# Optimization experiments

Hardware: AMD Instinct MI355X
Metric: run time of the kernel (lower is better)

Reference implementation:

```python
import jax, jax.numpy as jnp
import numpy as np

# irreps_in = irreps_out = 32x0e + 16x1o ; irreps_sh = 1x0e + 1x1o
MUL0, MUL1 = 32, 16
N_NODES = 12000
N_EDGES = 120000
INV_SQRT3 = float(1.0 / np.sqrt(3.0))   # w3j(1,1,0), w3j(0,1,1), w3j(1,0,1) coefficient
SQRT2 = float(np.sqrt(2.0))             # e3nn normalize2mom constant for ReLU
# e3nn TP norms: irrep_normalization='component', path_normalization='element'.
# Each output irrep receives paths with num_elements 32 and 16 -> x = 48.
N_0E = float(1.0 / np.sqrt(48.0))       # alpha = dim(0e)/48 = 1/48
N_1O = float(np.sqrt(3.0 / 48.0))       # alpha = dim(1o)/48 = 3/48
# uvw weight blocks (mul2 = 1): (s,y0->s),(s,y0->g),(v,y1->s),(v,y1->g),(s,y1->v),(v,y0->v)
SPLITS = [MUL0 * MUL0, MUL0 * MUL1, MUL1 * MUL0, MUL1 * MUL1, MUL0 * MUL1, MUL1 * MUL1]
OFFS = np.cumsum([0] + SPLITS)
WNUM = int(OFFS[-1])  # 3072


def setup_inputs() -> dict:
    key = jax.random.key(0)
    k1, k2, k3, k4, k5 = jax.random.split(key, 5)
    x = jax.random.normal(k1, (N_NODES, MUL0 + 3 * MUL1), dtype=jnp.float32)
    edge_attr = jax.random.normal(k2, (N_EDGES, 64), dtype=jnp.float32)
    Yij = jax.random.normal(k3, (N_EDGES, 4), dtype=jnp.float32)
    edge_index = jax.random.randint(k4, (2, N_EDGES), 0, N_NODES, dtype=jnp.int64)
    w_emb = jax.random.normal(k5, (2 * MUL0 + 64, WNUM), dtype=jnp.float32)
    return {"x": x, "edge_attr": edge_attr, "Yij": Yij,
            "edge_index": edge_index, "w_emb": w_emb}


def reference(x, edge_attr, Yij, edge_index, w_emb):
    dst, src = edge_index[0], edge_index[1]
    E = edge_attr.shape[0]
    xs = x[:, :MUL0]                                   # [N, 32] scalars (0e)
    xv = x[:, MUL0:].reshape(-1, MUL1, 3)              # [N, 16, 3] vectors (1o)

    # per-edge weight MLP (single e3nn FC layer, weight scaled by 1/sqrt(fan_in))
    emb = jnp.concatenate([xs[dst], xs[src], edge_attr], axis=-1)     # [E, 128]
    w = emb @ (w_emb / np.sqrt(w_emb.shape[0]))                       # [E, 3072]
    Ws = [w[:, OFFS[i]:OFFS[i + 1]] for i in range(6)]
    W1 = Ws[0].reshape(E, MUL0, MUL0)
    W2 = Ws[1].reshape(E, MUL0, MUL1)
    W3 = Ws[2].reshape(E, MUL1, MUL0)
    W4 = Ws[3].reshape(E, MUL1, MUL1)
    W5 = Ws[4].reshape(E, MUL0, MUL1)
    W6 = Ws[5].reshape(E, MUL1, MUL1)

    # gather source features, split sh
    x1s, x1v = xs[src], xv[src]                        # [E,32], [E,16,3]
    y0, y1 = Yij[:, 0], Yij[:, 1:4]                    # [E], [E,3]

    sy0 = x1s * y0[:, None]                            # 0e x 0e paths
    vdot = jnp.einsum('euk,ek->eu', x1v, y1) * INV_SQRT3  # 1o x 1o -> 0e
    out_s = N_0E * (jnp.einsum('euw,eu->ew', W1, sy0) +
                    jnp.einsum('euw,eu->ew', W3, vdot))    # [E, 32]
    out_g = N_0E * (jnp.einsum('euw,eu->ew', W2, sy0) +
                    jnp.einsum('euw,eu->ew', W4, vdot))    # [E, 16]
    out_v = (N_1O * INV_SQRT3) * (
        jnp.einsum('euw,eu,ek->ewk', W5, x1s, y1) +
        jnp.einsum('euw,euk->ewk', W6, x1v * y0[:, None, None]))  # [E, 16, 3]

    msg = jnp.concatenate([out_s, out_g, out_v.reshape(E, MUL1 * 3)], axis=-1)  # [E, 96]

    # scatter mean onto destination nodes
    summed = jax.ops.segment_sum(msg, dst, num_segments=N_NODES)
    cnt = jax.ops.segment_sum(jnp.ones((E,), msg.dtype), dst, num_segments=N_NODES)
    mean = summed / jnp.maximum(cnt, 1.0)[:, None]

    # Gate (e3nn Activation normalizes ReLU by sqrt(2))
    s = SQRT2 * jax.nn.relu(mean[:, :MUL0])
    g = SQRT2 * jax.nn.relu(mean[:, MUL0:MUL0 + MUL1])
    v = mean[:, MUL0 + MUL1:].reshape(-1, MUL1, 3) * g[:, :, None]
    out = jnp.concatenate([s, v.reshape(-1, MUL1 * 3)], axis=-1)     # [N, 80]
    return x + out
```

## Files before the change

### kernel.cpp

```cpp
#include <hip/hip_runtime.h>
#include <hip/hip_bf16.h>

#define E_EDGES 120000
#define NUM_NODES 12000

typedef __attribute__((ext_vector_type(8))) short bfrag;
typedef __attribute__((ext_vector_type(8))) unsigned short ushort8;
typedef __attribute__((ext_vector_type(4))) float f32x4;

#define INV_SQRT3 0.57735026918962576f
#define SQRT2_C   1.41421356237309515f
#define N_0E_C    0.14433756729740643f
#define NV_C      0.14433756729740643f
#define WSCALE    0.08838834764831845f

__device__ __forceinline__ unsigned short f2bf(float f) {
    union { float f; unsigned int u; } v; v.f = f;
    unsigned int r = v.u + 0x7fffu + ((v.u >> 16) & 1u);
    return (unsigned short)(r >> 16);
}

__device__ __forceinline__ ushort8 pack8(f32x4 a, f32x4 b) {
    ushort8 o;
    o[0] = f2bf(a.x); o[1] = f2bf(a.y); o[2] = f2bf(a.z); o[3] = f2bf(a.w);
    o[4] = f2bf(b.x); o[5] = f2bf(b.y); o[6] = f2bf(b.z); o[7] = f2bf(b.w);
    return o;
}

__global__ void k_wt(const float* __restrict__ w_emb, unsigned short* __restrict__ Bt) {
    int o = blockIdx.x * 256 + threadIdx.x;
    if (o >= 3072 * 128) return;
    int t = o >> 11;
    int c = (o >> 3) & 255;
    int j = o & 7;
    int kb = c >> 6;
    int quad = (c >> 4) & 3;
    int col = c & 15;
    int k = kb * 32 + quad * 8 + j;
    int n = t * 16 + col;
    Bt[o] = f2bf(w_emb[k * 3072 + n] * WSCALE);
}

__global__ void k_prep(const float* __restrict__ x, const float* __restrict__ edge_attr,
                       const float* __restrict__ Yij, const int* __restrict__ edge_index,
                       unsigned short* __restrict__ emb, float* __restrict__ rT,
                       float* __restrict__ cnt) {
    int e = blockIdx.x * 256 + threadIdx.x;
    if (e >= E_EDGES) return;
    int dst = edge_index[e];
    int src = edge_index[E_EDGES + e];
    f32x4 y = *(const f32x4*)(Yij + 4 * (long)e);
    float y0 = y.x, y1a = y.y, y1b = y.z, y1c = y.w;
    const float* xd = x + (long)dst * 80;
    const float* xs = x + (long)src * 80;
    const float* ea = edge_attr + (long)e * 64;

    ushort8* embp = (ushort8*)(emb + (long)e * 128);

    float xsv[80];
#pragma unroll
    for (int i = 0; i < 80; i += 4) {
        f32x4 v = *(const f32x4*)(xs + i);
        xsv[i] = v.x; xsv[i + 1] = v.y; xsv[i + 2] = v.z; xsv[i + 3] = v.w;
    }
#pragma unroll
    for (int cb = 0; cb < 4; ++cb) {
        f32x4 a = *(const f32x4*)(xd + cb * 8);
        f32x4 b = *(const f32x4*)(xd + cb * 8 + 4);
        embp[cb] = pack8(a, b);
    }
#pragma unroll
    for (int cb = 0; cb < 4; ++cb) {
        f32x4 a, b;
        a.x = xsv[cb * 8 + 0]; a.y = xsv[cb * 8 + 1]; a.z = xsv[cb * 8 + 2]; a.w = xsv[cb * 8 + 3];
        b.x = xsv[cb * 8 + 4]; b.y = xsv[cb * 8 + 5]; b.z = xsv[cb * 8 + 6]; b.w = xsv[cb * 8 + 7];
        embp[4 + cb] = pack8(a, b);
    }
#pragma unroll
    for (int cb = 0; cb < 8; ++cb) {
        f32x4 a = *(const f32x4*)(ea + cb * 8);
        f32x4 b = *(const f32x4*)(ea + cb * 8 + 4);
        embp[8 + cb] = pack8(a, b);
    }
#pragma unroll
    for (int u = 0; u < 32; ++u) rT[(long)u * E_EDGES + e] = xsv[u] * y0;
#pragma unroll
    for (int u = 0; u < 16; ++u)
        rT[(long)(32 + u) * E_EDGES + e] =
            (xsv[32 + 3 * u] * y1a + xsv[33 + 3 * u] * y1b + xsv[34 + 3 * u] * y1c) * INV_SQRT3;
#pragma unroll
    for (int u = 0; u < 32; ++u) rT[(long)(48 + u) * E_EDGES + e] = xsv[u];
#pragma unroll
    for (int j = 0; j < 48; ++j) rT[(long)(80 + j) * E_EDGES + e] = xsv[32 + j] * y0;
    atomicAdd(cnt + dst, 1.0f);
}

__global__ __launch_bounds__(256, 4) void k_gemm(
    const unsigned short* __restrict__ emb, const unsigned short* __restrict__ Bt,
    const float* __restrict__ rT, const int* __restrict__ edge_index,
    const float* __restrict__ Yij, float* __restrict__ summed) {
    const int lane = threadIdx.x & 63;
    const int wave = threadIdx.x >> 6;
    long e0 = (long)blockIdx.x * 128 + (long)wave * 32;
    const bool dup = (e0 + 32 > E_EDGES);
    if (dup) e0 = E_EDGES - 32;
    const int col = lane & 15, quad = lane >> 4;

    __shared__ __align__(16) char lds[2][16384];

    bfrag A[2][4];
#pragma unroll
    for (int s = 0; s < 2; ++s) {
        const unsigned short* ap = emb + (e0 + s * 16 + col) * 128 + quad * 8;
#pragma unroll
        for (int kb = 0; kb < 4; ++kb) A[s][kb] = *(const bfrag*)(ap + kb * 32);
    }

    auto stage = [&](int ci) {
        const char* g = (const char*)Bt + (size_t)ci * 16384 + wave * 4096 + lane * 16;
        char* l = &lds[ci & 1][wave * 4096];
#pragma unroll
        for (int j = 0; j < 4; ++j)
            __builtin_amdgcn_global_load_lds(
                (const __attribute__((address_space(1))) unsigned int*)(g + j * 1024),
                (__attribute__((address_space(3))) unsigned int*)(l + j * 1024), 16, 0, 0);
    };

    f32x4 z = {0.f, 0.f, 0.f, 0.f};
    f32x4 acc_s0[2] = {z, z}, acc_s1[2] = {z, z}, acc_g[2] = {z, z}, acc_t5[2] = {z, z};
    f32x4 acc_v[2][3] = {{z, z, z}, {z, z, z}};

    const float* rbase = rT + e0 + quad * 4;
    auto loadw = [&](int r, f32x4& a, f32x4& b) {
        const float* p = rbase + (long)r * E_EDGES;
        a = *(const f32x4*)(p);
        b = *(const f32x4*)(p + 16);
    };

    auto tile = [&](const char* lt, f32x4& c0, f32x4& c1) {
        bfrag B0 = *(const bfrag*)(lt + lane * 16);
        bfrag B1 = *(const bfrag*)(lt + lane * 16 + 1024);
        bfrag B2 = *(const bfrag*)(lt + lane * 16 + 2048);
        bfrag B3 = *(const bfrag*)(lt + lane * 16 + 3072);
        c0 = z; c1 = z;
        c0 = __builtin_amdgcn_mfma_f32_16x16x32_bf16(A[0][0], B0, c0, 0, 0, 0);
        c1 = __builtin_amdgcn_mfma_f32_16x16x32_bf16(A[1][0], B0, c1, 0, 0, 0);
        c0 = __builtin_amdgcn_mfma_f32_16x16x32_bf16(A[0][1], B1, c0, 0, 0, 0);
        c1 = __builtin_amdgcn_mfma_f32_16x16x32_bf16(A[1][1], B1, c1, 0, 0, 0);
        c0 = __builtin_amdgcn_mfma_f32_16x16x32_bf16(A[0][2], B2, c0, 0, 0, 0);
        c1 = __builtin_amdgcn_mfma_f32_16x16x32_bf16(A[1][2], B2, c1, 0, 0, 0);
        c0 = __builtin_amdgcn_mfma_f32_16x16x32_bf16(A[0][3], B3, c0, 0, 0, 0);
        c1 = __builtin_amdgcn_mfma_f32_16x16x32_bf16(A[1][3], B3, c1, 0, 0, 0);
    };

    stage(0);
    int cidx = 0;
    auto nextbuf = [&]() -> const char* {
        __syncthreads();
        if (cidx + 1 < 48) stage(cidx + 1);
        const char* b = lds[cidx & 1];
        ++cidx;
        return b;
    };

    f32x4 c0, c1;

    {
        f32x4 p0a, p0b, p1a, p1b;
        loadw(0, p0a, p0b); loadw(1, p1a, p1b);
#pragma unroll 1
        for (int j = 0; j < 16; ++j) {
            const char* buf = nextbuf();
            f32x4 w0a = p0a, w0b = p0b, w1a = p1a, w1b = p1b;
            int nr = (j < 15) ? (2 * j + 2) : 0;
            loadw(nr, p0a, p0b); loadw(nr + 1, p1a, p1b);
            tile(buf,         c0, c1); acc_s0[0] += c0 * w0a; acc_s0[1] += c1 * w0b;
            tile(buf + 4096,  c0, c1); acc_s1[0] += c0 * w0a; acc_s1[1] += c1 * w0b;
            tile(buf + 8192,  c0, c1); acc_s0[0] += c0 * w1a; acc_s0[1] += c1 * w1b;
            tile(buf + 12288, c0, c1); acc_s1[0] += c0 * w1a; acc_s1[1] += c1 * w1b;
        }
    }
    {
        f32x4 pa[4], pb[4];
#pragma unroll
        for (int i = 0; i < 4; ++i) loadw(i, pa[i], pb[i]);
#pragma unroll 1
        for (int j = 0; j < 8; ++j) {
            const char* buf = nextbuf();
            f32x4 wa[4], wb[4];
#pragma unroll
            for (int i = 0; i < 4; ++i) { wa[i] = pa[i]; wb[i] = pb[i]; }
            int nr = (j < 7) ? (4 * j + 4) : 0;
#pragma unroll
            for (int i = 0; i < 4; ++i) loadw(nr + i, pa[i], pb[i]);
#pragma unroll
            for (int i = 0; i < 4; ++i) {
                tile(buf + i * 4096, c0, c1);
                acc_g[0] += c0 * wa[i]; acc_g[1] += c1 * wb[i];
            }
        }
    }
    {
        f32x4 p0a, p0b, p1a, p1b;
        loadw(32, p0a, p0b); loadw(33, p1a, p1b);
#pragma unroll 1
        for (int j = 0; j < 8; ++j) {
            const char* buf = nextbuf();
            f32x4 w0a = p0a, w0b = p0b, w1a = p1a, w1b = p1b;
            int nr = (j < 7) ? (32 + 2 * j + 2) : 32;
            loadw(nr, p0a, p0b); loadw(nr + 1, p1a, p1b);
            tile(buf,         c0, c1); acc_s0[0] += c0 * w0a; acc_s0[1] += c1 * w0b;
            tile(buf + 4096,  c0, c1); acc_s1[0] += c0 * w0a; acc_s1[1] += c1 * w0b;
            tile(buf + 8192,  c0, c1); acc_s0[0] += c0 * w1a; acc_s0[1] += c1 * w1b;
            tile(buf + 12288, c0, c1); acc_s1[0] += c0 * w1a; acc_s1[1] += c1 * w1b;
        }
    }
    {
        f32x4 pa[4], pb[4];
#pragma unroll
        for (int i = 0; i < 4; ++i) loadw(32 + i, pa[i], pb[i]);
#pragma unroll 1
        for (int j = 0; j < 4; ++j) {
            const char* buf = nextbuf();
            f32x4 wa[4], wb[4];
#pragma unroll
            for (int i = 0; i < 4; ++i) { wa[i] = pa[i]; wb[i] = pb[i]; }
            int nr = (j < 3) ? (32 + 4 * j + 4) : 32;
#pragma unroll
            for (int i = 0; i < 4; ++i) loadw(nr + i, pa[i], pb[i]);
#pragma unroll
            for (int i = 0; i < 4; ++i) {
                tile(buf + i * 4096, c0, c1);
                acc_g[0] += c0 * wa[i]; acc_g[1] += c1 * wb[i];
            }
        }
    }
    {
        f32x4 pa[4], pb[4];
#pragma unroll
        for (int i = 0; i < 4; ++i) loadw(48 + i, pa[i], pb[i]);
#pragma unroll 1
        for (int j = 0; j < 8; ++j) {
            const char* buf = nextbuf();
            f32x4 wa[4], wb[4];
#pragma unroll
            for (int i = 0; i < 4; ++i) { wa[i] = pa[i]; wb[i] = pb[i]; }
            int nr = (j < 7) ? (48 + 4 * j + 4) : 48;
#pragma unroll
            for (int i = 0; i < 4; ++i) loadw(nr + i, pa[i], pb[i]);
#pragma unroll
            for (int i = 0; i < 4; ++i) {
                tile(buf + i * 4096, c0, c1);
                acc_t5[0] += c0 * wa[i]; acc_t5[1] += c1 * wb[i];
            }
        }
    }
    {
        f32x4 va[3], vb[3];
#pragma unroll
        for (int k = 0; k < 3; ++k) loadw(80 + k, va[k], vb[k]);
#pragma unroll 1
        for (int j = 0; j < 4; ++j) {
            const char* buf = nextbuf();
#pragma unroll
            for (int i = 0; i < 4; ++i) {
                f32x4 wa[3], wb[3];
#pragma unroll
                for (int k = 0; k < 3; ++k) { wa[k] = va[k]; wb[k] = vb[k]; }
                int un = 4 * j + i + 1; if (un > 15) un = 0;
#pragma unroll
                for (int k = 0; k < 3; ++k) loadw(80 + 3 * un + k, va[k], vb[k]);
                tile(buf + i * 4096, c0, c1);
#pragma unroll
                for (int k = 0; k < 3; ++k) {
                    acc_v[0][k] += c0 * wa[k];
                    acc_v[1][k] += c1 * wb[k];
                }
            }
        }
    }

    if (dup) return;
#pragma unroll
    for (int s = 0; s < 2; ++s) {
        long eb = e0 + s * 16 + quad * 4;
#pragma unroll
        for (int r = 0; r < 4; ++r) {
            long e = eb + r;
            int d = edge_index[e];
            float* base = summed + (long)d * 96;
            float y1a = Yij[4 * e + 1], y1b = Yij[4 * e + 2], y1c = Yij[4 * e + 3];
            atomicAdd(base + col,       N_0E_C * acc_s0[s][r]);
            atomicAdd(base + col + 16,  N_0E_C * acc_s1[s][r]);
            atomicAdd(base + 32 + col,  N_0E_C * acc_g[s][r]);
            float t5 = acc_t5[s][r];
            atomicAdd(base + 48 + col * 3 + 0, NV_C * (t5 * y1a + acc_v[s][0][r]));
            atomicAdd(base + 48 + col * 3 + 1, NV_C * (t5 * y1b + acc_v[s][1][r]));
            atomicAdd(base + 48 + col * 3 + 2, NV_C * (t5 * y1c + acc_v[s][2][r]));
        }
    }
}

__global__ void k_final(const float* __restrict__ x, const float* __restrict__ summed,
                        const float* __restrict__ cnt, float* __restrict__ out) {
    int tid = blockIdx.x * 256 + threadIdx.x;
    if (tid >= NUM_NODES * 80) return;
    int n = tid / 80, c = tid % 80;
    float m = fmaxf(cnt[n], 1.0f);
    float inv = 1.0f / m;
    float val;
    if (c < 32) {
        val = SQRT2_C * fmaxf(summed[(long)n * 96 + c] * inv, 0.0f);
    } else {
        int j = c - 32;
        int w = j / 3;
        float g = SQRT2_C * fmaxf(summed[(long)n * 96 + 32 + w] * inv, 0.0f);
        val = summed[(long)n * 96 + 48 + j] * inv * g;
    }
    out[tid] = x[tid] + val;
}

extern "C" void kernel_launch(void* const* d_in, const int* in_sizes, int n_in,
                              void* d_out, int out_size, void* d_ws, size_t ws_size,
                              hipStream_t stream) {
    const float* x         = (const float*)d_in[0];
    const float* edge_attr = (const float*)d_in[1];
    const float* Yij       = (const float*)d_in[2];
    const int*   edge_index= (const int*)d_in[3];
    const float* w_emb     = (const float*)d_in[4];
    float* out = (float*)d_out;

    char* ws = (char*)d_ws;
    size_t off = 0;
    unsigned short* emb = (unsigned short*)(ws + off); off += (size_t)E_EDGES * 128 * 2;
    unsigned short* Bt  = (unsigned short*)(ws + off); off += (size_t)3072 * 128 * 2;
    off = (off + 255) & ~(size_t)255;
    float* rT     = (float*)(ws + off); off += (size_t)128 * E_EDGES * 4;
    size_t zoff = off;
    float* summed = (float*)(ws + off); off += (size_t)NUM_NODES * 96 * 4;
    float* cnt    = (float*)(ws + off); off += (size_t)NUM_NODES * 4;

    hipMemsetAsync(ws + zoff, 0, (size_t)NUM_NODES * 97 * 4, stream);
    k_wt  <<<(3072 * 128 + 255) / 256, 256, 0, stream>>>(w_emb, Bt);
    k_prep<<<(E_EDGES + 255) / 256, 256, 0, stream>>>(x, edge_attr, Yij, edge_index, emb, rT, cnt);
    k_gemm<<<(E_EDGES + 127) / 128, 256, 0, stream>>>(emb, Bt, rT, edge_index, Yij, summed);
    k_final<<<(NUM_NODES * 80 + 255) / 256, 256, 0, stream>>>(x, summed, cnt, out);
}
```

Before: 299.3 us.

## Factor y0 out of per-edge weights and stage weight rows in LDS

Moves the y0 multiplication out of the precomputed per-edge rows and applies it once per output in the epilogue, using separate accumulators for each weight block. This removes duplicate rows and shrinks the rT buffer from 128 to 96 rows, which cuts both the write traffic in k_prep and the read traffic in k_gemm. Each block now bulk-loads its 96x128 slice of rT into LDS with global_load_lds instead of issuing per-iteration prefetched global loads. The extra 48KB of LDS forces launch bounds down from 4 to 2 blocks per CU, so the kernel has less latency hiding. It also needs more accumulator registers.

Result: slower. 306.1 us (+2.3%).

```diff
diff --git a/kernel.cpp b/kernel.cpp
--- a/kernel.cpp
+++ b/kernel.cpp
@@ -50,7 +50,7 @@
     int dst = edge_index[e];
     int src = edge_index[E_EDGES + e];
     f32x4 y = *(const f32x4*)(Yij + 4 * (long)e);
-    float y0 = y.x, y1a = y.y, y1b = y.z, y1c = y.w;
+    float y1a = y.y, y1b = y.z, y1c = y.w;
     const float* xd = x + (long)dst * 80;
     const float* xs = x + (long)src * 80;
     const float* ea = edge_attr + (long)e * 64;
@@ -83,19 +83,17 @@
         embp[8 + cb] = pack8(a, b);
     }
 #pragma unroll
-    for (int u = 0; u < 32; ++u) rT[(long)u * E_EDGES + e] = xsv[u] * y0;
+    for (int u = 0; u < 32; ++u) rT[(long)u * E_EDGES + e] = xsv[u];
 #pragma unroll
     for (int u = 0; u < 16; ++u)
         rT[(long)(32 + u) * E_EDGES + e] =
             (xsv[32 + 3 * u] * y1a + xsv[33 + 3 * u] * y1b + xsv[34 + 3 * u] * y1c) * INV_SQRT3;
 #pragma unroll
-    for (int u = 0; u < 32; ++u) rT[(long)(48 + u) * E_EDGES + e] = xsv[u];
-#pragma unroll
-    for (int j = 0; j < 48; ++j) rT[(long)(80 + j) * E_EDGES + e] = xsv[32 + j] * y0;
+    for (int j = 0; j < 48; ++j) rT[(long)(48 + j) * E_EDGES + e] = xsv[32 + j];
     atomicAdd(cnt + dst, 1.0f);
 }
 
-__global__ __launch_bounds__(256, 4) void k_gemm(
+__global__ __launch_bounds__(256, 2) void k_gemm(
     const unsigned short* __restrict__ emb, const unsigned short* __restrict__ Bt,
     const float* __restrict__ rT, const int* __restrict__ edge_index,
     const float* __restrict__ Yij, float* __restrict__ summed) {
@@ -107,6 +105,7 @@
     const int col = lane & 15, quad = lane >> 4;
 
     __shared__ __align__(16) char lds[2][16384];
+    __shared__ __align__(16) float wlds[96][128];
 
     bfrag A[2][4];
 #pragma unroll
@@ -114,6 +113,21 @@
         const unsigned short* ap = emb + (e0 + s * 16 + col) * 128 + quad * 8;
 #pragma unroll
         for (int kb = 0; kb < 4; ++kb) A[s][kb] = *(const bfrag*)(ap + kb * 32);
+    }
+
+    {
+#pragma unroll
+        for (int it = 0; it < 12; ++it) {
+            int o = it * 4096 + wave * 1024 + lane * 16;
+            int row = o >> 9;
+            int rb = o & 511;
+            const char* g = (const char*)rT + (size_t)row * ((size_t)E_EDGES * 4)
+                          + (size_t)blockIdx.x * 512 + rb;
+            char* l = (char*)wlds + it * 4096 + wave * 1024;
+            __builtin_amdgcn_global_load_lds(
+                (const __attribute__((address_space(1))) unsigned int*)g,
+                (__attribute__((address_space(3))) unsigned int*)l, 16, 0, 0);
+        }
     }
 
     auto stage = [&](int ci) {
@@ -127,14 +141,16 @@
     };
 
     f32x4 z = {0.f, 0.f, 0.f, 0.f};
-    f32x4 acc_s0[2] = {z, z}, acc_s1[2] = {z, z}, acc_g[2] = {z, z}, acc_t5[2] = {z, z};
+    f32x4 accW1_0[2] = {z, z}, accW1_1[2] = {z, z};
+    f32x4 accW3_0[2] = {z, z}, accW3_1[2] = {z, z};
+    f32x4 accW2[2] = {z, z}, accW4[2] = {z, z};
+    f32x4 acc_t5[2] = {z, z};
     f32x4 acc_v[2][3] = {{z, z, z}, {z, z, z}};
 
-    const float* rbase = rT + e0 + quad * 4;
+    const int woff = wave * 32 + quad * 4;
     auto loadw = [&](int r, f32x4& a, f32x4& b) {
-        const float* p = rbase + (long)r * E_EDGES;
-        a = *(const f32x4*)(p);
-        b = *(const f32x4*)(p + 16);
+        a = *(const f32x4*)&wlds[r][woff];
+        b = *(const f32x4*)&wlds[r][woff + 16];
     };
 
     auto tile = [&](const char* lt, f32x4& c0, f32x4& c1) {
@@ -165,117 +181,67 @@
 
     f32x4 c0, c1;
 
-    {
-        f32x4 p0a, p0b, p1a, p1b;
-        loadw(0, p0a, p0b); loadw(1, p1a, p1b);
-#pragma unroll 1
-        for (int j = 0; j < 16; ++j) {
-            const char* buf = nextbuf();
-            f32x4 w0a = p0a, w0b = p0b, w1a = p1a, w1b = p1b;
-            int nr = (j < 15) ? (2 * j + 2) : 0;
-            loadw(nr, p0a, p0b); loadw(nr + 1, p1a, p1b);
-            tile(buf,         c0, c1); acc_s0[0] += c0 * w0a; acc_s0[1] += c1 * w0b;
-            tile(buf + 4096,  c0, c1); acc_s1[0] += c0 * w0a; acc_s1[1] += c1 * w0b;
-            tile(buf + 8192,  c0, c1); acc_s0[0] += c0 * w1a; acc_s0[1] += c1 * w1b;
-            tile(buf + 12288, c0, c1); acc_s1[0] += c0 * w1a; acc_s1[1] += c1 * w1b;
-        }
-    }
-    {
-        f32x4 pa[4], pb[4];
-#pragma unroll
-        for (int i = 0; i < 4; ++i) loadw(i, pa[i], pb[i]);
-#pragma unroll 1
-        for (int j = 0; j < 8; ++j) {
-            const char* buf = nextbuf();
-            f32x4 wa[4], wb[4];
-#pragma unroll
-            for (int i = 0; i < 4; ++i) { wa[i] = pa[i]; wb[i] = pb[i]; }
-            int nr = (j < 7) ? (4 * j + 4) : 0;
-#pragma unroll
-            for (int i = 0; i < 4; ++i) loadw(nr + i, pa[i], pb[i]);
-#pragma unroll
-            for (int i = 0; i < 4; ++i) {
-                tile(buf + i * 4096, c0, c1);
-                acc_g[0] += c0 * wa[i]; acc_g[1] += c1 * wb[i];
-            }
-        }
-    }
-    {
-        f32x4 p0a, p0b, p1a, p1b;
-        loadw(32, p0a, p0b); loadw(33, p1a, p1b);
-#pragma unroll 1
-        for (int j = 0; j < 8; ++j) {
-            const char* buf = nextbuf();
-            f32x4 w0a = p0a, w0b = p0b, w1a = p1a, w1b = p1b;
-            int nr = (j < 7) ? (32 + 2 * j + 2) : 32;
-            loadw(nr, p0a, p0b); loadw(nr + 1, p1a, p1b);
-            tile(buf,         c0, c1); acc_s0[0] += c0 * w0a; acc_s0[1] += c1 * w0b;
-            tile(buf + 4096,  c0, c1); acc_s1[0] += c0 * w0a; acc_s1[1] += c1 * w0b;
-            tile(buf + 8192,  c0, c1); acc_s0[0] += c0 * w1a; acc_s0[1] += c1 * w1b;
-            tile(buf + 12288, c0, c1); acc_s1[0] += c0 * w1a; acc_s1[1] += c1 * w1b;
-        }
-    }
-    {
-        f32x4 pa[4], pb[4];
-#pragma unroll
-        for (int i = 0; i < 4; ++i) loadw(32 + i, pa[i], pb[i]);
-#pragma unroll 1
-        for (int j = 0; j < 4; ++j) {
-            const char* buf = nextbuf();
-            f32x4 wa[4], wb[4];
-#pragma unroll
-            for (int i = 0; i < 4; ++i) { wa[i] = pa[i]; wb[i] = pb[i]; }
-            int nr = (j < 3) ? (32 + 4 * j + 4) : 32;
-#pragma unroll
-            for (int i = 0; i < 4; ++i) loadw(nr + i, pa[i], pb[i]);
-#pragma unroll
-            for (int i = 0; i < 4; ++i) {
-                tile(buf + i * 4096, c0, c1);
-                acc_g[0] += c0 * wa[i]; acc_g[1] += c1 * wb[i];
-            }
-        }
-    }
-    {
-        f32x4 pa[4], pb[4];
-#pragma unroll
-        for (int i = 0; i < 4; ++i) loadw(48 + i, pa[i], pb[i]);
-#pragma unroll 1
-        for (int j = 0; j < 8; ++j) {
-            const char* buf = nextbuf();
-            f32x4 wa[4], wb[4];
-#pragma unroll
-            for (int i = 0; i < 4; ++i) { wa[i] = pa[i]; wb[i] = pb[i]; }
-            int nr = (j < 7) ? (48 + 4 * j + 4) : 48;
-#pragma unroll
-            for (int i = 0; i < 4; ++i) loadw(nr + i, pa[i], pb[i]);
-#pragma unroll
-            for (int i = 0; i < 4; ++i) {
-                tile(buf + i * 4096, c0, c1);
-                acc_t5[0] += c0 * wa[i]; acc_t5[1] += c1 * wb[i];
-            }
-        }
-    }
-    {
-        f32x4 va[3], vb[3];
-#pragma unroll
-        for (int k = 0; k < 3; ++k) loadw(80 + k, va[k], vb[k]);
-#pragma unroll 1
-        for (int j = 0; j < 4; ++j) {
-            const char* buf = nextbuf();
-#pragma unroll
-            for (int i = 0; i < 4; ++i) {
-                f32x4 wa[3], wb[3];
-#pragma unroll
-                for (int k = 0; k < 3; ++k) { wa[k] = va[k]; wb[k] = vb[k]; }
-                int un = 4 * j + i + 1; if (un > 15) un = 0;
-#pragma unroll
-                for (int k = 0; k < 3; ++k) loadw(80 + 3 * un + k, va[k], vb[k]);
-                tile(buf + i * 4096, c0, c1);
-#pragma unroll
-                for (int k = 0; k < 3; ++k) {
-                    acc_v[0][k] += c0 * wa[k];
-                    acc_v[1][k] += c1 * wb[k];
-                }
+#pragma unroll 1
+    for (int j = 0; j < 16; ++j) {
+        const char* buf = nextbuf();
+        f32x4 w0a, w0b, w1a, w1b;
+        loadw(2 * j, w0a, w0b); loadw(2 * j + 1, w1a, w1b);
+        tile(buf,         c0, c1); accW1_0[0] += c0 * w0a; accW1_0[1] += c1 * w0b;
+        tile(buf + 4096,  c0, c1); accW1_1[0] += c0 * w0a; accW1_1[1] += c1 * w0b;
+        tile(buf + 8192,  c0, c1); accW1_0[0] += c0 * w1a; accW1_0[1] += c1 * w1b;
+        tile(buf + 12288, c0, c1); accW1_1[0] += c0 * w1a; accW1_1[1] += c1 * w1b;
+    }
+#pragma unroll 1
+    for (int j = 0; j < 8; ++j) {
+        const char* buf = nextbuf();
+#pragma unroll
+        for (int i = 0; i < 4; ++i) {
+            f32x4 wa, wb; loadw(4 * j + i, wa, wb);
+            tile(buf + i * 4096, c0, c1);
+            accW2[0] += c0 * wa; accW2[1] += c1 * wb;
+        }
+    }
+#pragma unroll 1
+    for (int j = 0; j < 8; ++j) {
+        const char* buf = nextbuf();
+        f32x4 w0a, w0b, w1a, w1b;
+        loadw(32 + 2 * j, w0a, w0b); loadw(32 + 2 * j + 1, w1a, w1b);
+        tile(buf,         c0, c1); accW3_0[0] += c0 * w0a; accW3_0[1] += c1 * w0b;
+        tile(buf + 4096,  c0, c1); accW3_1[0] += c0 * w0a; accW3_1[1] += c1 * w0b;
+        tile(buf + 8192,  c0, c1); accW3_0[0] += c0 * w1a; accW3_0[1] += c1 * w1b;
+        tile(buf + 12288, c0, c1); accW3_1[0] += c0 * w1a; accW3_1[1] += c1 * w1b;
+    }
+#pragma unroll 1
+    for (int j = 0; j < 4; ++j) {
+        const char* buf = nextbuf();
+#pragma unroll
+        for (int i = 0; i < 4; ++i) {
+            f32x4 wa, wb; loadw(32 + 4 * j + i, wa, wb);
+            tile(buf + i * 4096, c0, c1);
+            accW4[0] += c0 * wa; accW4[1] += c1 * wb;
+        }
+    }
+#pragma unroll 1
+    for (int j = 0; j < 8; ++j) {
+        const char* buf = nextbuf();
+#pragma unroll
+        for (int i = 0; i < 4; ++i) {
+            f32x4 wa, wb; loadw(4 * j + i, wa, wb);
+            tile(buf + i * 4096, c0, c1);
+            acc_t5[0] += c0 * wa; acc_t5[1] += c1 * wb;
+        }
+    }
+#pragma unroll 1
+    for (int j = 0; j < 4; ++j) {
+        const char* buf = nextbuf();
+#pragma unroll
+        for (int i = 0; i < 4; ++i) {
+            int u = 4 * j + i;
+            tile(buf + i * 4096, c0, c1);
+#pragma unroll
+            for (int k = 0; k < 3; ++k) {
+                f32x4 wa, wb; loadw(48 + 3 * u + k, wa, wb);
+                acc_v[0][k] += c0 * wa; acc_v[1][k] += c1 * wb;
             }
         }
     }
@@ -289,14 +255,15 @@
             long e = eb + r;
             int d = edge_index[e];
             float* base = summed + (long)d * 96;
-            float y1a = Yij[4 * e + 1], y1b = Yij[4 * e + 2], y1c = Yij[4 * e + 3];
-            atomicAdd(base + col,       N_0E_C * acc_s0[s][r]);
-            atomicAdd(base + col + 16,  N_0E_C * acc_s1[s][r]);
-            atomicAdd(base + 32 + col,  N_0E_C * acc_g[s][r]);
+            f32x4 y = *(const f32x4*)(Yij + 4 * e);
+            float y0 = y.x, y1a = y.y, y1b = y.z, y1c = y.w;
+            atomicAdd(base + col,      N_0E_C * (y0 * accW1_0[s][r] + accW3_0[s][r]));
+            atomicAdd(base + col + 16, N_0E_C * (y0 * accW1_1[s][r] + accW3_1[s][r]));
+            atomicAdd(base + 32 + col, N_0E_C * (y0 * accW2[s][r] + accW4[s][r]));
             float t5 = acc_t5[s][r];
-            atomicAdd(base + 48 + col * 3 + 0, NV_C * (t5 * y1a + acc_v[s][0][r]));
-            atomicAdd(base + 48 + col * 3 + 1, NV_C * (t5 * y1b + acc_v[s][1][r]));
-            atomicAdd(base + 48 + col * 3 + 2, NV_C * (t5 * y1c + acc_v[s][2][r]));
+            atomicAdd(base + 48 + col * 3 + 0, NV_C * (t5 * y1a + y0 * acc_v[s][0][r]));
+            atomicAdd(base + 48 + col * 3 + 1, NV_C * (t5 * y1b + y0 * acc_v[s][1][r]));
+            atomicAdd(base + 48 + col * 3 + 2, NV_C * (t5 * y1c + y0 * acc_v[s][2][r]));
         }
     }
 }
@@ -335,7 +302,7 @@
     unsigned short* emb = (unsigned short*)(ws + off); off += (size_t)E_EDGES * 128 * 2;
     unsigned short* Bt  = (unsigned short*)(ws + off); off += (size_t)3072 * 128 * 2;
     off = (off + 255) & ~(size_t)255;
-    float* rT     = (float*)(ws + off); off += (size_t)128 * E_EDGES * 4;
+    float* rT     = (float*)(ws + off); off += (size_t)96 * E_EDGES * 4;
     size_t zoff = off;
     float* summed = (float*)(ws + off); off += (size_t)NUM_NODES * 96 * 4;
     float* cnt    = (float*)(ws + off); off += (size_t)NUM_NODES * 4;
```

## Prefetch LDS chunks two ahead with split barriers and MFMA priority

Applied to the files above, without the earlier changes.

Reworks the double-buffered LDS pipeline. Each chunk now waits with a partial vmcnt before one barrier, then re-stages the freed buffer two chunks ahead after a second barrier. The goal is for global-to-LDS copies to overlap more of the MFMA work, instead of a full syncthreads followed immediately by staging. It also raises wave priority around the MFMA tile sections with s_setprio. The price is a second barrier per chunk and hand-tuned waitcnt values that depend on how many loads are in flight.

Result: slower. 449.6 us (+50.2%).

```diff
diff --git a/kernel.cpp b/kernel.cpp
--- a/kernel.cpp
+++ b/kernel.cpp
@@ -153,31 +153,41 @@
         c1 = __builtin_amdgcn_mfma_f32_16x16x32_bf16(A[1][3], B3, c1, 0, 0, 0);
     };
 
+    int cidx = 0;
+    auto chunk_top = [&]() -> const char* {
+        asm volatile("s_waitcnt vmcnt(4)" ::: "memory");
+        __builtin_amdgcn_s_barrier();
+        asm volatile("" ::: "memory");
+        return lds[cidx & 1];
+    };
+    auto chunk_bot = [&]() {
+        __builtin_amdgcn_s_setprio(0);
+        asm volatile("" ::: "memory");
+        __builtin_amdgcn_s_barrier();
+        asm volatile("" ::: "memory");
+        if (cidx + 2 < 48) stage(cidx + 2);
+        ++cidx;
+    };
+
+    f32x4 c0, c1;
+
     stage(0);
-    int cidx = 0;
-    auto nextbuf = [&]() -> const char* {
-        __syncthreads();
-        if (cidx + 1 < 48) stage(cidx + 1);
-        const char* b = lds[cidx & 1];
-        ++cidx;
-        return b;
-    };
-
-    f32x4 c0, c1;
-
     {
         f32x4 p0a, p0b, p1a, p1b;
         loadw(0, p0a, p0b); loadw(1, p1a, p1b);
+        stage(1);
 #pragma unroll 1
         for (int j = 0; j < 16; ++j) {
-            const char* buf = nextbuf();
+            const char* buf = chunk_top();
             f32x4 w0a = p0a, w0b = p0b, w1a = p1a, w1b = p1b;
             int nr = (j < 15) ? (2 * j + 2) : 0;
             loadw(nr, p0a, p0b); loadw(nr + 1, p1a, p1b);
+            __builtin_amdgcn_s_setprio(1);
             tile(buf,         c0, c1); acc_s0[0] += c0 * w0a; acc_s0[1] += c1 * w0b;
             tile(buf + 4096,  c0, c1); acc_s1[0] += c0 * w0a; acc_s1[1] += c1 * w0b;
             tile(buf + 8192,  c0, c1); acc_s0[0] += c0 * w1a; acc_s0[1] += c1 * w1b;
             tile(buf + 12288, c0, c1); acc_s1[0] += c0 * w1a; acc_s1[1] += c1 * w1b;
+            chunk_bot();
         }
     }
     {
@@ -186,18 +196,20 @@
         for (int i = 0; i < 4; ++i) loadw(i, pa[i], pb[i]);
 #pragma unroll 1
         for (int j = 0; j < 8; ++j) {
-            const char* buf = nextbuf();
+            const char* buf = chunk_top();
             f32x4 wa[4], wb[4];
 #pragma unroll
             for (int i = 0; i < 4; ++i) { wa[i] = pa[i]; wb[i] = pb[i]; }
             int nr = (j < 7) ? (4 * j + 4) : 0;
 #pragma unroll
             for (int i = 0; i < 4; ++i) loadw(nr + i, pa[i], pb[i]);
+            __builtin_amdgcn_s_setprio(1);
 #pragma unroll
             for (int i = 0; i < 4; ++i) {
                 tile(buf + i * 4096, c0, c1);
                 acc_g[0] += c0 * wa[i]; acc_g[1] += c1 * wb[i];
             }
+            chunk_bot();
         }
     }
     {
@@ -205,14 +217,16 @@
         loadw(32, p0a, p0b); loadw(33, p1a, p1b);
 #pragma unroll 1
         for (int j = 0; j < 8; ++j) {
-            const char* buf = nextbuf();
+            const char* buf = chunk_top();
             f32x4 w0a = p0a, w0b = p0b, w1a = p1a, w1b = p1b;
             int nr = (j < 7) ? (32 + 2 * j + 2) : 32;
             loadw(nr, p0a, p0b); loadw(nr + 1, p1a, p1b);
+            __builtin_amdgcn_s_setprio(1);
             tile(buf,         c0, c1); acc_s0[0] += c0 * w0a; acc_s0[1] += c1 * w0b;
             tile(buf + 4096,  c0, c1); acc_s1[0] += c0 * w0a; acc_s1[1] += c1 * w0b;
             tile(buf + 8192,  c0, c1); acc_s0[0] += c0 * w1a; acc_s0[1] += c1 * w1b;
             tile(buf + 12288, c0, c1); acc_s1[0] += c0 * w1a; acc_s1[1] += c1 * w1b;
+            chunk_bot();
         }
     }
     {
@@ -221,18 +235,20 @@
         for (int i = 0; i < 4; ++i) loadw(32 + i, pa[i], pb[i]);
 #pragma unroll 1
         for (int j = 0; j < 4; ++j) {
-            const char* buf = nextbuf();
+            const char* buf = chunk_top();
             f32x4 wa[4], wb[4];
 #pragma unroll
             for (int i = 0; i < 4; ++i) { wa[i] = pa[i]; wb[i] = pb[i]; }
             int nr = (j < 3) ? (32 + 4 * j + 4) : 32;
 #pragma unroll
             for (int i = 0; i < 4; ++i) loadw(nr + i, pa[i], pb[i]);
+            __builtin_amdgcn_s_setprio(1);
 #pragma unroll
             for (int i = 0; i < 4; ++i) {
                 tile(buf + i * 4096, c0, c1);
                 acc_g[0] += c0 * wa[i]; acc_g[1] += c1 * wb[i];
             }
+            chunk_bot();
         }
     }
     {
@@ -241,18 +257,20 @@
         for (int i = 0; i < 4; ++i) loadw(48 + i, pa[i], pb[i]);
 #pragma unroll 1
         for (int j = 0; j < 8; ++j) {
-            const char* buf = nextbuf();
+            const char* buf = chunk_top();
             f32x4 wa[4], wb[4];
 #pragma unroll
             for (int i = 0; i < 4; ++i) { wa[i] = pa[i]; wb[i] = pb[i]; }
             int nr = (j < 7) ? (48 + 4 * j + 4) : 48;
 #pragma unroll
             for (int i = 0; i < 4; ++i) loadw(nr + i, pa[i], pb[i]);
+            __builtin_amdgcn_s_setprio(1);
 #pragma unroll
             for (int i = 0; i < 4; ++i) {
                 tile(buf + i * 4096, c0, c1);
                 acc_t5[0] += c0 * wa[i]; acc_t5[1] += c1 * wb[i];
             }
+            chunk_bot();
         }
     }
     {
@@ -261,7 +279,7 @@
         for (int k = 0; k < 3; ++k) loadw(80 + k, va[k], vb[k]);
 #pragma unroll 1
         for (int j = 0; j < 4; ++j) {
-            const char* buf = nextbuf();
+            const char* buf = chunk_top();
 #pragma unroll
             for (int i = 0; i < 4; ++i) {
                 f32x4 wa[3], wb[3];
@@ -270,13 +288,16 @@
                 int un = 4 * j + i + 1; if (un > 15) un = 0;
 #pragma unroll
                 for (int k = 0; k < 3; ++k) loadw(80 + 3 * un + k, va[k], vb[k]);
+                __builtin_amdgcn_s_setprio(1);
                 tile(buf + i * 4096, c0, c1);
 #pragma unroll
                 for (int k = 0; k < 3; ++k) {
                     acc_v[0][k] += c0 * wa[k];
                     acc_v[1][k] += c1 * wb[k];
                 }
+                __builtin_amdgcn_s_setprio(0);
             }
+            chunk_bot();
         }
     }
 
```

## Sort edges by destination and remap gemm blocks per XCD for atomic locality

Applied to the files above, without the earlier changes.

Adds a counting sort of edges by destination node (count, single-block scan, scatter), so prep and gemm process edges in dst-sorted order. The scatter-add atomics into summed then hit contiguous node rows, and consecutive blocks are remapped so each XCD handles a contiguous range of edges, improving L2 locality of the atomics. The cost is three extra small kernels (one of them a serial single-block scan), extra workspace, and gathered reads of edge_attr and Yij via the permutation. Y values are also staged in sorted order for the epilogue.

Result: slower. 450.3 us (+50.5%).

```diff
diff --git a/kernel.cpp b/kernel.cpp
--- a/kernel.cpp
+++ b/kernel.cpp
@@ -41,21 +41,59 @@
     Bt[o] = f2bf(w_emb[k * 3072 + n] * WSCALE);
 }
 
+__global__ void k_count(const int* __restrict__ edge_index, float* __restrict__ cnt) {
+    int e = blockIdx.x * 256 + threadIdx.x;
+    if (e >= E_EDGES) return;
+    atomicAdd(cnt + edge_index[e], 1.0f);
+}
+
+__global__ void k_scan(const float* __restrict__ cnt, int* __restrict__ offs) {
+    __shared__ int psum[256];
+    int t = threadIdx.x;
+    const int SEG = (NUM_NODES + 255) / 256;
+    int lo = t * SEG;
+    int hi = lo + SEG; if (hi > NUM_NODES) hi = NUM_NODES;
+    int s = 0;
+    for (int i = lo; i < hi; ++i) s += (int)cnt[i];
+    psum[t] = s;
+    __syncthreads();
+    if (t == 0) {
+        int acc = 0;
+        for (int i = 0; i < 256; ++i) { int v = psum[i]; psum[i] = acc; acc += v; }
+    }
+    __syncthreads();
+    int acc = psum[t];
+    for (int i = lo; i < hi; ++i) { offs[i] = acc; acc += (int)cnt[i]; }
+}
+
+__global__ void k_scatter(const int* __restrict__ edge_index, const int* __restrict__ offs,
+                          int* __restrict__ cursor, int* __restrict__ perm_src,
+                          int* __restrict__ dsts) {
+    int e = blockIdx.x * 256 + threadIdx.x;
+    if (e >= E_EDGES) return;
+    int d = edge_index[e];
+    int p = offs[d] + atomicAdd(cursor + d, 1);
+    perm_src[p] = e;
+    dsts[p] = d;
+}
+
 __global__ void k_prep(const float* __restrict__ x, const float* __restrict__ edge_attr,
                        const float* __restrict__ Yij, const int* __restrict__ edge_index,
+                       const int* __restrict__ perm_src, const int* __restrict__ dsts,
                        unsigned short* __restrict__ emb, float* __restrict__ rT,
-                       float* __restrict__ cnt) {
-    int e = blockIdx.x * 256 + threadIdx.x;
-    if (e >= E_EDGES) return;
-    int dst = edge_index[e];
-    int src = edge_index[E_EDGES + e];
-    f32x4 y = *(const f32x4*)(Yij + 4 * (long)e);
+                       f32x4* __restrict__ ys) {
+    int p = blockIdx.x * 256 + threadIdx.x;
+    if (p >= E_EDGES) return;
+    int eid = perm_src[p];
+    int dst = dsts[p];
+    int src = edge_index[E_EDGES + eid];
+    f32x4 y = *(const f32x4*)(Yij + 4 * (long)eid);
     float y0 = y.x, y1a = y.y, y1b = y.z, y1c = y.w;
     const float* xd = x + (long)dst * 80;
     const float* xs = x + (long)src * 80;
-    const float* ea = edge_attr + (long)e * 64;
-
-    ushort8* embp = (ushort8*)(emb + (long)e * 128);
+    const float* ea = edge_attr + (long)eid * 64;
+
+    ushort8* embp = (ushort8*)(emb + (long)p * 128);
 
     float xsv[80];
 #pragma unroll
@@ -83,25 +121,30 @@
         embp[8 + cb] = pack8(a, b);
     }
 #pragma unroll
-    for (int u = 0; u < 32; ++u) rT[(long)u * E_EDGES + e] = xsv[u] * y0;
+    for (int u = 0; u < 32; ++u) rT[(long)u * E_EDGES + p] = xsv[u] * y0;
 #pragma unroll
     for (int u = 0; u < 16; ++u)
-        rT[(long)(32 + u) * E_EDGES + e] =
+        rT[(long)(32 + u) * E_EDGES + p] =
             (xsv[32 + 3 * u] * y1a + xsv[33 + 3 * u] * y1b + xsv[34 + 3 * u] * y1c) * INV_SQRT3;
 #pragma unroll
-    for (int u = 0; u < 32; ++u) rT[(long)(48 + u) * E_EDGES + e] = xsv[u];
-#pragma unroll
-    for (int j = 0; j < 48; ++j) rT[(long)(80 + j) * E_EDGES + e] = xsv[32 + j] * y0;
-    atomicAdd(cnt + dst, 1.0f);
+    for (int u = 0; u < 32; ++u) rT[(long)(48 + u) * E_EDGES + p] = xsv[u];
+#pragma unroll
+    for (int j = 0; j < 48; ++j) rT[(long)(80 + j) * E_EDGES + p] = xsv[32 + j] * y0;
+    ys[p] = y;
 }
 
 __global__ __launch_bounds__(256, 4) void k_gemm(
     const unsigned short* __restrict__ emb, const unsigned short* __restrict__ Bt,
-    const float* __restrict__ rT, const int* __restrict__ edge_index,
-    const float* __restrict__ Yij, float* __restrict__ summed) {
+    const float* __restrict__ rT, const int* __restrict__ dsts,
+    const f32x4* __restrict__ ys, float* __restrict__ summed) {
     const int lane = threadIdx.x & 63;
     const int wave = threadIdx.x >> 6;
-    long e0 = (long)blockIdx.x * 128 + (long)wave * 32;
+    const int NB = (E_EDGES + 127) / 128;
+    const int q = NB >> 3, r = NB & 7;
+    int hb = blockIdx.x;
+    int xcd = hb & 7, ii = hb >> 3;
+    int lb = (xcd < r ? xcd * (q + 1) : r * (q + 1) + (xcd - r) * q) + ii;
+    long e0 = (long)lb * 128 + (long)wave * 32;
     const bool dup = (e0 + 32 > E_EDGES);
     if (dup) e0 = E_EDGES - 32;
     const int col = lane & 15, quad = lane >> 4;
@@ -131,8 +174,8 @@
     f32x4 acc_v[2][3] = {{z, z, z}, {z, z, z}};
 
     const float* rbase = rT + e0 + quad * 4;
-    auto loadw = [&](int r, f32x4& a, f32x4& b) {
-        const float* p = rbase + (long)r * E_EDGES;
+    auto loadw = [&](int r_, f32x4& a, f32x4& b) {
+        const float* p = rbase + (long)r_ * E_EDGES;
         a = *(const f32x4*)(p);
         b = *(const f32x4*)(p + 16);
     };
@@ -285,18 +328,19 @@
     for (int s = 0; s < 2; ++s) {
         long eb = e0 + s * 16 + quad * 4;
 #pragma unroll
-        for (int r = 0; r < 4; ++r) {
-            long e = eb + r;
-            int d = edge_index[e];
+        for (int r_ = 0; r_ < 4; ++r_) {
+            long e = eb + r_;
+            int d = dsts[e];
             float* base = summed + (long)d * 96;
-            float y1a = Yij[4 * e + 1], y1b = Yij[4 * e + 2], y1c = Yij[4 * e + 3];
-            atomicAdd(base + col,       N_0E_C * acc_s0[s][r]);
-            atomicAdd(base + col + 16,  N_0E_C * acc_s1[s][r]);
-            atomicAdd(base + 32 + col,  N_0E_C * acc_g[s][r]);
-            float t5 = acc_t5[s][r];
-            atomicAdd(base + 48 + col * 3 + 0, NV_C * (t5 * y1a + acc_v[s][0][r]));
-            atomicAdd(base + 48 + col * 3 + 1, NV_C * (t5 * y1b + acc_v[s][1][r]));
-            atomicAdd(base + 48 + col * 3 + 2, NV_C * (t5 * y1c + acc_v[s][2][r]));
+            f32x4 y = ys[e];
+            float y1a = y.y, y1b = y.z, y1c = y.w;
+            atomicAdd(base + col,       N_0E_C * acc_s0[s][r_]);
+            atomicAdd(base + col + 16,  N_0E_C * acc_s1[s][r_]);
+            atomicAdd(base + 32 + col,  N_0E_C * acc_g[s][r_]);
+            float t5 = acc_t5[s][r_];
+            atomicAdd(base + 48 + col * 3 + 0, NV_C * (t5 * y1a + acc_v[s][0][r_]));
+            atomicAdd(base + 48 + col * 3 + 1, NV_C * (t5 * y1b + acc_v[s][1][r_]));
+            atomicAdd(base + 48 + col * 3 + 2, NV_C * (t5 * y1c + acc_v[s][2][r_]));
         }
     }
 }
@@ -335,14 +379,23 @@
     unsigned short* emb = (unsigned short*)(ws + off); off += (size_t)E_EDGES * 128 * 2;
     unsigned short* Bt  = (unsigned short*)(ws + off); off += (size_t)3072 * 128 * 2;
     off = (off + 255) & ~(size_t)255;
-    float* rT     = (float*)(ws + off); off += (size_t)128 * E_EDGES * 4;
+    float* rT      = (float*)(ws + off); off += (size_t)128 * E_EDGES * 4;
+    f32x4* ys      = (f32x4*)(ws + off); off += (size_t)E_EDGES * 16;
+    int*   perm_src= (int*)(ws + off);   off += (size_t)E_EDGES * 4;
+    int*   dsts    = (int*)(ws + off);   off += (size_t)E_EDGES * 4;
+    int*   offs    = (int*)(ws + off);   off += (size_t)NUM_NODES * 4;
     size_t zoff = off;
-    float* summed = (float*)(ws + off); off += (size_t)NUM_NODES * 96 * 4;
-    float* cnt    = (float*)(ws + off); off += (size_t)NUM_NODES * 4;
-
-    hipMemsetAsync(ws + zoff, 0, (size_t)NUM_NODES * 97 * 4, stream);
-    k_wt  <<<(3072 * 128 + 255) / 256, 256, 0, stream>>>(w_emb, Bt);
-    k_prep<<<(E_EDGES + 255) / 256, 256, 0, stream>>>(x, edge_attr, Yij, edge_index, emb, rT, cnt);
-    k_gemm<<<(E_EDGES + 127) / 128, 256, 0, stream>>>(emb, Bt, rT, edge_index, Yij, summed);
-    k_final<<<(NUM_NODES * 80 + 255) / 256, 256, 0, stream>>>(x, summed, cnt, out);
-}
+    float* summed  = (float*)(ws + off); off += (size_t)NUM_NODES * 96 * 4;
+    float* cnt     = (float*)(ws + off); off += (size_t)NUM_NODES * 4;
+    int*   cursor  = (int*)(ws + off);   off += (size_t)NUM_NODES * 4;
+
+    hipMemsetAsync(ws + zoff, 0, (size_t)NUM_NODES * 98 * 4, stream);
+    k_wt     <<<(3072 * 128 + 255) / 256, 256, 0, stream>>>(w_emb, Bt);
+    k_count  <<<(E_EDGES + 255) / 256, 256, 0, stream>>>(edge_index, cnt);
+    k_scan   <<<1, 256, 0, stream>>>(cnt, offs);
+    k_scatter<<<(E_EDGES + 255) / 256, 256, 0, stream>>>(edge_index, offs, cursor, perm_src, dsts);
+    k_prep   <<<(E_EDGES + 255) / 256, 256, 0, stream>>>(x, edge_attr, Yij, edge_index,
+                                                         perm_src, dsts, emb, rT, ys);
+    k_gemm   <<<(E_EDGES + 127) / 128, 256, 0, stream>>>(emb, Bt, rT, dsts, ys, summed);
+    k_final  <<<(NUM_NODES * 80 + 255) / 256, 256, 0, stream>>>(x, summed, cnt, out);
+}
```
